# Optimization experiments

Measured on AMD Instinct MI355X. Metric: run time of the kernel, lower is better.

The kernel has to match this reference:

```python
import jax, jax.numpy as jnp
import numpy as np

HEAD_DIM = 16

def setup_inputs() -> dict:
    key = jax.random.key(0)
    ks = jax.random.split(key, 6)
    b, m, n, e, k, d = 2, 2048, 2048, 128, 8, HEAD_DIM
    # xavier-uniform-like scale for [e, d] fan
    s = float(np.sqrt(6.0 / (e + d)))
    return {
        "x": jax.random.normal(ks[0], (b, m, e), dtype=jnp.float32),
        "y": jax.random.normal(ks[1], (b, n, e), dtype=jnp.float32),
        "lambda1": jax.random.uniform(ks[2], (k, e, d), jnp.float32, -s, s),
        "lambda2": jax.random.uniform(ks[3], (k, e, d), jnp.float32, -s, s),
        "theta1": jax.random.uniform(ks[4], (k, e, d), jnp.float32, -s, s),
        "theta2": jax.random.uniform(ks[5], (k, e, d), jnp.float32, -s, s),
        "bias_lambda": jnp.zeros((k, d), jnp.float32),
        "bias_theta": jnp.zeros((k, d), jnp.float32),
    }

def reference(x, y, lambda1, lambda2, theta1, theta2, bias_lambda, bias_theta):
    head_dim = lambda1.shape[-1]
    # r: [b, m, k, d]
    r = jnp.einsum('bmp,kpd->bmkd', x, lambda1) + bias_lambda
    # dot_att: [k, b, m, n] (bilinear QK via per-head projections of x and y)
    dot_att = jnp.einsum('bmkd,kqd,bnq->kbmn', r, lambda2, y)
    dot_att = dot_att * (head_dim ** -0.5)
    # softmax over the query/m axis (-2), NOT the key axis
    att = jax.nn.softmax(dot_att, axis=-2)
    # combine: [b, n, k, d]
    r2 = jnp.einsum('kbmn,bmp,kpd->bnkd', att, x, theta1) + bias_theta
    # output: [b, n, emb_dim_x]
    return jnp.einsum('bnkd,kqd->bnq', r2, theta2)
```

## Files before the change

kernel.cpp:

```cpp
#include <hip/hip_runtime.h>
#include <math.h>

#define BB 2
#define MM 2048
#define NN 2048
#define EE 128
#define KH 8
#define DD 16
#define NHEADS (BB * KH)
#define MSPLIT 4
#define MCHUNK (MM / MSPLIT)

typedef __bf16 bf16x8 __attribute__((ext_vector_type(8)));
typedef __bf16 bf16x4 __attribute__((ext_vector_type(4)));
typedef float  f32x16 __attribute__((ext_vector_type(16)));
typedef float  f32x4  __attribute__((ext_vector_type(4)));

__global__ __launch_bounds__(256) void proj_kernel(
    const float* __restrict__ x, const float* __restrict__ y,
    const float* __restrict__ lambda1, const float* __restrict__ lambda2,
    const float* __restrict__ theta1, const float* __restrict__ bias_lambda,
    __bf16* __restrict__ rK, __bf16* __restrict__ kyQ, __bf16* __restrict__ Vt)
{
    __shared__ float xs[16][132];
    __shared__ float Ws[128][16];
    __shared__ float ts[16][17];

    const int tile = blockIdx.x;
    const int mt = tile & 127;
    const int k  = (tile >> 7) & 7;
    const int b  = tile >> 10;
    const int f  = blockIdx.y;
    const int tid = threadIdx.x;
    const int head = b * KH + k;

    const float* src = (f == 2) ? y : x;
    const float* W   = (f == 0) ? lambda1 : ((f == 1) ? theta1 : lambda2);

    const float* sp = src + ((size_t)b * MM + (size_t)mt * 16) * EE;
    for (int i = tid; i < 512; i += 256) {
        float4 v = ((const float4*)sp)[i];
        int row = i >> 5, cp = (i & 31) * 4;
        *(float4*)&xs[row][cp] = v;
    }
    const float* wp = W + (size_t)k * (EE * DD);
    for (int i = tid; i < 512; i += 256) {
        float4 v = ((const float4*)wp)[i];
        int row = i >> 2, cp = (i & 3) * 4;
        *(float4*)&Ws[row][cp] = v;
    }
    __syncthreads();

    const int row = tid >> 4, col = tid & 15;
    float acc = (f == 0) ? bias_lambda[k * DD + col] : 0.0f;
    #pragma unroll 16
    for (int p = 0; p < EE; ++p)
        acc = fmaf(xs[row][p], Ws[p][col], acc);

    const int m = mt * 16 + row;
    if (f == 0) {
        rK[((size_t)head * MM + m) * DD + col] = (__bf16)acc;
    } else if (f == 2) {
        kyQ[((size_t)head * NN + m) * DD + col] = (__bf16)(acc * 0.25f);
    } else {
        ts[col][row] = acc;
        __syncthreads();
        const int dd2 = tid >> 4, mloc = tid & 15;
        Vt[((size_t)head * DD + dd2) * MM + mt * 16 + mloc] = (__bf16)ts[dd2][mloc];
    }
}

__global__ __launch_bounds__(256) void attn_kernel(
    const __bf16* __restrict__ rK, const __bf16* __restrict__ kyQ,
    const __bf16* __restrict__ Vt,
    float* __restrict__ Opart, float* __restrict__ mlP)
{
    __shared__ __bf16 Pst[4][32][40];

    const int tid  = threadIdx.x;
    const int wave = tid >> 6;
    const int lane = tid & 63;
    const int head = blockIdx.x >> 4;
    const int nbase = (blockIdx.x & 15) * 128 + wave * 32;
    const int ms   = blockIdx.y;

    const int l31 = lane & 31;
    const int hi  = lane >> 5;
    const int l15 = lane & 15;
    const int g4  = lane >> 4;

    const bf16x8 qf = *reinterpret_cast<const bf16x8*>(
        kyQ + ((size_t)head * NN + nbase + l31) * DD + 8 * hi);

    f32x4 o0, o1;
    #pragma unroll
    for (int i = 0; i < 4; ++i) { o0[i] = 0.f; o1[i] = 0.f; }
    float mmax = -INFINITY, lsum = 0.f;

    const __bf16* kb = rK + (size_t)head * MM * DD;
    const __bf16* vb = Vt + (size_t)head * DD * MM;

    for (int it = 0; it < MCHUNK / 32; ++it) {
        const int m0 = ms * MCHUNK + it * 32;

        const bf16x8 kf = *reinterpret_cast<const bf16x8*>(
            kb + ((size_t)(m0 + l31)) * DD + 8 * hi);

        f32x16 s;
        #pragma unroll
        for (int i = 0; i < 16; ++i) s[i] = 0.f;
        s = __builtin_amdgcn_mfma_f32_32x32x16_bf16(kf, qf, s, 0, 0, 0);

        float tm = s[0];
        #pragma unroll
        for (int r = 1; r < 16; ++r) tm = fmaxf(tm, s[r]);
        tm = fmaxf(tm, __shfl_xor(tm, 32));
        const float newm = fmaxf(mmax, tm);
        const float c = __expf(mmax - newm);

        float p[16];
        float ps = 0.f;
        #pragma unroll
        for (int r = 0; r < 16; ++r) { p[r] = __expf(s[r] - newm); ps += p[r]; }
        ps += __shfl_xor(ps, 32);
        lsum = lsum * c + ps;
        mmax = newm;

        #pragma unroll
        for (int qd = 0; qd < 4; ++qd) {
            bf16x4 pk;
            pk[0] = (__bf16)p[4 * qd + 0];
            pk[1] = (__bf16)p[4 * qd + 1];
            pk[2] = (__bf16)p[4 * qd + 2];
            pk[3] = (__bf16)p[4 * qd + 3];
            *reinterpret_cast<bf16x4*>(&Pst[wave][l31][8 * qd + 4 * hi]) = pk;
        }

        const bf16x8 vf = *reinterpret_cast<const bf16x8*>(
            vb + (size_t)l15 * MM + m0 + 8 * g4);

        const bf16x8 pa0 = *reinterpret_cast<const bf16x8*>(&Pst[wave][l15][8 * g4]);
        const bf16x8 pa1 = *reinterpret_cast<const bf16x8*>(&Pst[wave][16 + l15][8 * g4]);

        #pragma unroll
        for (int r = 0; r < 4; ++r) {
            const float c0 = __shfl(c, 4 * g4 + r);
            const float c1 = __shfl(c, 16 + 4 * g4 + r);
            o0[r] *= c0;
            o1[r] *= c1;
        }
        o0 = __builtin_amdgcn_mfma_f32_16x16x32_bf16(pa0, vf, o0, 0, 0, 0);
        o1 = __builtin_amdgcn_mfma_f32_16x16x32_bf16(pa1, vf, o1, 0, 0, 0);
    }

    float* obase = Opart + ((size_t)ms * NHEADS + head) * NN * DD;
    #pragma unroll
    for (int r = 0; r < 4; ++r) {
        const int n0 = nbase + 4 * g4 + r;
        const int n1 = n0 + 16;
        obase[(size_t)n0 * DD + l15] = o0[r];
        obase[(size_t)n1 * DD + l15] = o1[r];
    }
    if (lane < 32) {
        const size_t mlbase = (((size_t)ms * NHEADS + head) * NN + nbase + l31) * 2;
        mlP[mlbase]     = mmax;
        mlP[mlbase + 1] = lsum;
    }
}

__global__ __launch_bounds__(256) void combine_kernel(
    const float* __restrict__ Opart, const float* __restrict__ mlP,
    const float* __restrict__ bias_theta, const float* __restrict__ theta2,
    float* __restrict__ out)
{
    __shared__ float r2s[2][128];

    const int pairIdx = blockIdx.x;
    const int b   = pairIdx >> 10;
    const int np0 = (pairIdx & 1023) * 2;
    const int tid = threadIdx.x;

    {
        const int n_loc = tid >> 7;
        const int rem = tid & 127;
        const int k = rem >> 4, dd = rem & 15;
        const int n = np0 + n_loc;
        const int head = b * KH + k;

        float mm[MSPLIT], ls[MSPLIT];
        float Mx = -INFINITY;
        #pragma unroll
        for (int s2 = 0; s2 < MSPLIT; ++s2) {
            const size_t base = ((size_t)s2 * NHEADS + head) * NN + n;
            mm[s2] = mlP[base * 2];
            ls[s2] = mlP[base * 2 + 1];
            Mx = fmaxf(Mx, mm[s2]);
        }
        float L = 0.f, O = 0.f;
        #pragma unroll
        for (int s2 = 0; s2 < MSPLIT; ++s2) {
            const float w = __expf(mm[s2] - Mx);
            L += ls[s2] * w;
            O = fmaf(Opart[(((size_t)s2 * NHEADS + head) * NN + n) * DD + dd], w, O);
        }
        r2s[n_loc][rem] = O / L + bias_theta[k * DD + dd];
    }
    __syncthreads();
    {
        const int n_loc = tid >> 7;
        const int qq = tid & 127;
        const int n = np0 + n_loc;
        float acc = 0.f;
        #pragma unroll
        for (int k = 0; k < KH; ++k) {
            const float4* t2 = (const float4*)(theta2 + ((size_t)k * EE + qq) * DD);
            const float* r2p = &r2s[n_loc][k * DD];
            float4 t0 = t2[0], t1 = t2[1], t2v = t2[2], t3 = t2[3];
            acc = fmaf(r2p[0],  t0.x, acc); acc = fmaf(r2p[1],  t0.y, acc);
            acc = fmaf(r2p[2],  t0.z, acc); acc = fmaf(r2p[3],  t0.w, acc);
            acc = fmaf(r2p[4],  t1.x, acc); acc = fmaf(r2p[5],  t1.y, acc);
            acc = fmaf(r2p[6],  t1.z, acc); acc = fmaf(r2p[7],  t1.w, acc);
            acc = fmaf(r2p[8],  t2v.x, acc); acc = fmaf(r2p[9],  t2v.y, acc);
            acc = fmaf(r2p[10], t2v.z, acc); acc = fmaf(r2p[11], t2v.w, acc);
            acc = fmaf(r2p[12], t3.x, acc); acc = fmaf(r2p[13], t3.y, acc);
            acc = fmaf(r2p[14], t3.z, acc); acc = fmaf(r2p[15], t3.w, acc);
        }
        out[((size_t)b * NN + n) * EE + qq] = acc;
    }
}

extern "C" void kernel_launch(void* const* d_in, const int* in_sizes, int n_in,
                              void* d_out, int out_size, void* d_ws, size_t ws_size,
                              hipStream_t stream) {
    const float* x           = (const float*)d_in[0];
    const float* y           = (const float*)d_in[1];
    const float* lambda1     = (const float*)d_in[2];
    const float* lambda2     = (const float*)d_in[3];
    const float* theta1      = (const float*)d_in[4];
    const float* theta2      = (const float*)d_in[5];
    const float* bias_lambda = (const float*)d_in[6];
    const float* bias_theta  = (const float*)d_in[7];
    float* out = (float*)d_out;

    char* w = (char*)d_ws;
    __bf16* rK  = (__bf16*)w;  w += (size_t)NHEADS * MM * DD * 2;
    __bf16* kyQ = (__bf16*)w;  w += (size_t)NHEADS * NN * DD * 2;
    __bf16* Vt  = (__bf16*)w;  w += (size_t)NHEADS * DD * MM * 2;
    float* Opart = (float*)w;  w += (size_t)MSPLIT * NHEADS * NN * DD * 4;
    float* mlP   = (float*)w;

    hipLaunchKernelGGL(proj_kernel, dim3(2048, 3), dim3(256), 0, stream,
                       x, y, lambda1, lambda2, theta1, bias_lambda, rK, kyQ, Vt);
    hipLaunchKernelGGL(attn_kernel, dim3(256, MSPLIT), dim3(256), 0, stream,
                       rK, kyQ, Vt, Opart, mlP);
    hipLaunchKernelGGL(combine_kernel, dim3(2048), dim3(256), 0, stream,
                       Opart, mlP, bias_theta, theta2, out);
}
```

Measured before the change: 130.9 us.

## Rewrite projection with MFMA, defer softmax rescale, double M-split, relayout partials

The projection kernel now runs on bf16 MFMA instructions, with each wave handling several 16-row tiles, replacing the scalar LDS FMA loop. The attention kernel uses exp2 with log2e folded into the query scale. It also skips rescaling the running max and accumulators unless the new max exceeds the old by more than a threshold. MSPLIT goes from 4 to 8 for more parallelism, and the partial outputs are relaid out as [split, b, n, k, d] so the combine kernel can use float4 loads and handle four rows per block. Risks: bf16 rounding of x and the weights in the projection, a deferred max that lets exponents reach up to 2^8, and twice as much partial-output traffic.

After: 116.3 us. 11.2% less time.

```diff
diff --git a/kernel.cpp b/kernel.cpp
--- a/kernel.cpp
+++ b/kernel.cpp
@@ -8,13 +8,23 @@
 #define KH 8
 #define DD 16
 #define NHEADS (BB * KH)
-#define MSPLIT 4
+#define MSPLIT 8
 #define MCHUNK (MM / MSPLIT)
+#define LOG2E 1.44269504088896340736f
+#define QSCALE (0.25f * LOG2E)
+#define DEFER_THR 8.0f
 
 typedef __bf16 bf16x8 __attribute__((ext_vector_type(8)));
 typedef __bf16 bf16x4 __attribute__((ext_vector_type(4)));
 typedef float  f32x16 __attribute__((ext_vector_type(16)));
 typedef float  f32x4  __attribute__((ext_vector_type(4)));
+
+__device__ inline bf16x8 cvt8(float4 a, float4 b) {
+    bf16x8 r;
+    r[0] = (__bf16)a.x; r[1] = (__bf16)a.y; r[2] = (__bf16)a.z; r[3] = (__bf16)a.w;
+    r[4] = (__bf16)b.x; r[5] = (__bf16)b.y; r[6] = (__bf16)b.z; r[7] = (__bf16)b.w;
+    return r;
+}
 
 __global__ __launch_bounds__(256) void proj_kernel(
     const float* __restrict__ x, const float* __restrict__ y,
@@ -22,51 +32,59 @@
     const float* __restrict__ theta1, const float* __restrict__ bias_lambda,
     __bf16* __restrict__ rK, __bf16* __restrict__ kyQ, __bf16* __restrict__ Vt)
 {
-    __shared__ float xs[16][132];
-    __shared__ float Ws[128][16];
-    __shared__ float ts[16][17];
-
-    const int tile = blockIdx.x;
-    const int mt = tile & 127;
-    const int k  = (tile >> 7) & 7;
-    const int b  = tile >> 10;
-    const int f  = blockIdx.y;
-    const int tid = threadIdx.x;
-    const int head = b * KH + k;
-
-    const float* src = (f == 2) ? y : x;
-    const float* W   = (f == 0) ? lambda1 : ((f == 1) ? theta1 : lambda2);
-
-    const float* sp = src + ((size_t)b * MM + (size_t)mt * 16) * EE;
-    for (int i = tid; i < 512; i += 256) {
-        float4 v = ((const float4*)sp)[i];
-        int row = i >> 5, cp = (i & 31) * 4;
-        *(float4*)&xs[row][cp] = v;
-    }
-    const float* wp = W + (size_t)k * (EE * DD);
-    for (int i = tid; i < 512; i += 256) {
-        float4 v = ((const float4*)wp)[i];
-        int row = i >> 2, cp = (i & 3) * 4;
-        *(float4*)&Ws[row][cp] = v;
-    }
-    __syncthreads();
-
-    const int row = tid >> 4, col = tid & 15;
-    float acc = (f == 0) ? bias_lambda[k * DD + col] : 0.0f;
-    #pragma unroll 16
-    for (int p = 0; p < EE; ++p)
-        acc = fmaf(xs[row][p], Ws[p][col], acc);
-
-    const int m = mt * 16 + row;
-    if (f == 0) {
-        rK[((size_t)head * MM + m) * DD + col] = (__bf16)acc;
-    } else if (f == 2) {
-        kyQ[((size_t)head * NN + m) * DD + col] = (__bf16)(acc * 0.25f);
-    } else {
-        ts[col][row] = acc;
-        __syncthreads();
-        const int dd2 = tid >> 4, mloc = tid & 15;
-        Vt[((size_t)head * DD + dd2) * MM + mt * 16 + mloc] = (__bf16)ts[dd2][mloc];
+    const int grp  = blockIdx.x;
+    const int f    = blockIdx.y;
+    const int head = blockIdx.z;
+    const int b = head >> 3, kh = head & 7;
+    const int wave = threadIdx.x >> 6;
+    const int lane = threadIdx.x & 63;
+    const int l15 = lane & 15, g4 = lane >> 4;
+
+    const float* W   = ((f == 0) ? lambda1 : (f == 1) ? theta1 : lambda2)
+                       + (size_t)kh * EE * DD;
+    const float* src = ((f == 2) ? y : x) + (size_t)b * MM * EE;
+
+    bf16x8 wf[4];
+    #pragma unroll
+    for (int kb = 0; kb < 4; ++kb) {
+        const float* wp = W + (size_t)(32 * kb + 8 * g4) * DD + l15;
+        bf16x8 t;
+        #pragma unroll
+        for (int e = 0; e < 8; ++e) t[e] = (__bf16)wp[e * DD];
+        wf[kb] = t;
+    }
+    const float bl = (f == 0) ? bias_lambda[kh * DD + l15] : 0.f;
+
+    for (int i = 0; i < 4; ++i) {
+        const int m0 = (grp * 16 + wave * 4 + i) * 16;
+        const float* xp = src + (size_t)(m0 + l15) * EE + 8 * g4;
+
+        f32x4 acc;
+        #pragma unroll
+        for (int r = 0; r < 4; ++r) acc[r] = 0.f;
+
+        #pragma unroll
+        for (int kb = 0; kb < 4; ++kb) {
+            float4 a = *(const float4*)(xp + 32 * kb);
+            float4 c = *(const float4*)(xp + 32 * kb + 4);
+            bf16x8 xf = cvt8(a, c);
+            if (f == 1) acc = __builtin_amdgcn_mfma_f32_16x16x32_bf16(wf[kb], xf, acc, 0, 0, 0);
+            else        acc = __builtin_amdgcn_mfma_f32_16x16x32_bf16(xf, wf[kb], acc, 0, 0, 0);
+        }
+
+        if (f == 0) {
+            #pragma unroll
+            for (int r = 0; r < 4; ++r)
+                rK[((size_t)head * MM + m0 + 4 * g4 + r) * DD + l15] = (__bf16)(acc[r] + bl);
+        } else if (f == 2) {
+            #pragma unroll
+            for (int r = 0; r < 4; ++r)
+                kyQ[((size_t)head * NN + m0 + 4 * g4 + r) * DD + l15] = (__bf16)(acc[r] * QSCALE);
+        } else {
+            #pragma unroll
+            for (int r = 0; r < 4; ++r)
+                Vt[((size_t)head * DD + 4 * g4 + r) * MM + m0 + l15] = (__bf16)acc[r];
+        }
     }
 }
 
@@ -83,6 +101,7 @@
     const int head = blockIdx.x >> 4;
     const int nbase = (blockIdx.x & 15) * 128 + wave * 32;
     const int ms   = blockIdx.y;
+    const int b = head >> 3, kh = head & 7;
 
     const int l31 = lane & 31;
     const int hi  = lane >> 5;
@@ -115,16 +134,25 @@
         #pragma unroll
         for (int r = 1; r < 16; ++r) tm = fmaxf(tm, s[r]);
         tm = fmaxf(tm, __shfl_xor(tm, 32));
-        const float newm = fmaxf(mmax, tm);
-        const float c = __expf(mmax - newm);
+
+        if (!__all(tm - mmax <= DEFER_THR)) {
+            const float newm = fmaxf(mmax, tm);
+            const float c = exp2f(mmax - newm);
+            lsum *= c;
+            #pragma unroll
+            for (int r = 0; r < 4; ++r) {
+                o0[r] *= __shfl(c, 4 * g4 + r);
+                o1[r] *= __shfl(c, 16 + 4 * g4 + r);
+            }
+            mmax = newm;
+        }
 
         float p[16];
         float ps = 0.f;
         #pragma unroll
-        for (int r = 0; r < 16; ++r) { p[r] = __expf(s[r] - newm); ps += p[r]; }
+        for (int r = 0; r < 16; ++r) { p[r] = exp2f(s[r] - mmax); ps += p[r]; }
         ps += __shfl_xor(ps, 32);
-        lsum = lsum * c + ps;
-        mmax = newm;
+        lsum += ps;
 
         #pragma unroll
         for (int qd = 0; qd < 4; ++qd) {
@@ -142,27 +170,20 @@
         const bf16x8 pa0 = *reinterpret_cast<const bf16x8*>(&Pst[wave][l15][8 * g4]);
         const bf16x8 pa1 = *reinterpret_cast<const bf16x8*>(&Pst[wave][16 + l15][8 * g4]);
 
-        #pragma unroll
-        for (int r = 0; r < 4; ++r) {
-            const float c0 = __shfl(c, 4 * g4 + r);
-            const float c1 = __shfl(c, 16 + 4 * g4 + r);
-            o0[r] *= c0;
-            o1[r] *= c1;
-        }
         o0 = __builtin_amdgcn_mfma_f32_16x16x32_bf16(pa0, vf, o0, 0, 0, 0);
         o1 = __builtin_amdgcn_mfma_f32_16x16x32_bf16(pa1, vf, o1, 0, 0, 0);
     }
 
-    float* obase = Opart + ((size_t)ms * NHEADS + head) * NN * DD;
+    float* obase = Opart + (((size_t)ms * BB + b) * NN) * (KH * DD) + kh * DD;
     #pragma unroll
     for (int r = 0; r < 4; ++r) {
         const int n0 = nbase + 4 * g4 + r;
         const int n1 = n0 + 16;
-        obase[(size_t)n0 * DD + l15] = o0[r];
-        obase[(size_t)n1 * DD + l15] = o1[r];
+        obase[(size_t)n0 * (KH * DD) + l15] = o0[r];
+        obase[(size_t)n1 * (KH * DD) + l15] = o1[r];
     }
     if (lane < 32) {
-        const size_t mlbase = (((size_t)ms * NHEADS + head) * NN + nbase + l31) * 2;
+        const size_t mlbase = (((size_t)ms * BB + b) * NN + nbase + l31) * (KH * 2) + kh * 2;
         mlP[mlbase]     = mmax;
         mlP[mlbase + 1] = lsum;
     }
@@ -173,59 +194,71 @@
     const float* __restrict__ bias_theta, const float* __restrict__ theta2,
     float* __restrict__ out)
 {
-    __shared__ float r2s[2][128];
-
-    const int pairIdx = blockIdx.x;
-    const int b   = pairIdx >> 10;
-    const int np0 = (pairIdx & 1023) * 2;
+    __shared__ float r2s[4][128];
+
+    const int blk = blockIdx.x;
+    const int b   = blk >> 9;
+    const int n0  = (blk & 511) * 4;
     const int tid = threadIdx.x;
 
-    {
-        const int n_loc = tid >> 7;
-        const int rem = tid & 127;
-        const int k = rem >> 4, dd = rem & 15;
-        const int n = np0 + n_loc;
-        const int head = b * KH + k;
+    if (tid < 128) {
+        const int n_loc = tid >> 5;
+        const int k  = (tid >> 2) & 7;
+        const int dq = tid & 3;
+        const int n = n0 + n_loc;
 
         float mm[MSPLIT], ls[MSPLIT];
         float Mx = -INFINITY;
         #pragma unroll
-        for (int s2 = 0; s2 < MSPLIT; ++s2) {
-            const size_t base = ((size_t)s2 * NHEADS + head) * NN + n;
-            mm[s2] = mlP[base * 2];
-            ls[s2] = mlP[base * 2 + 1];
-            Mx = fmaxf(Mx, mm[s2]);
-        }
-        float L = 0.f, O = 0.f;
-        #pragma unroll
-        for (int s2 = 0; s2 < MSPLIT; ++s2) {
-            const float w = __expf(mm[s2] - Mx);
-            L += ls[s2] * w;
-            O = fmaf(Opart[(((size_t)s2 * NHEADS + head) * NN + n) * DD + dd], w, O);
-        }
-        r2s[n_loc][rem] = O / L + bias_theta[k * DD + dd];
+        for (int s = 0; s < MSPLIT; ++s) {
+            const size_t base = (((size_t)s * BB + b) * NN + n) * (KH * 2) + k * 2;
+            mm[s] = mlP[base];
+            ls[s] = mlP[base + 1];
+            Mx = fmaxf(Mx, mm[s]);
+        }
+        float L = 0.f;
+        float4 O = make_float4(0.f, 0.f, 0.f, 0.f);
+        #pragma unroll
+        for (int s = 0; s < MSPLIT; ++s) {
+            const float w = exp2f(mm[s] - Mx);
+            L = fmaf(ls[s], w, L);
+            const float4 op = *(const float4*)(
+                Opart + (((size_t)s * BB + b) * NN + n) * (KH * DD) + k * DD + dq * 4);
+            O.x = fmaf(w, op.x, O.x); O.y = fmaf(w, op.y, O.y);
+            O.z = fmaf(w, op.z, O.z); O.w = fmaf(w, op.w, O.w);
+        }
+        const float inv = 1.f / L;
+        const float* bt = bias_theta + k * DD + dq * 4;
+        float4 res;
+        res.x = fmaf(O.x, inv, bt[0]);
+        res.y = fmaf(O.y, inv, bt[1]);
+        res.z = fmaf(O.z, inv, bt[2]);
+        res.w = fmaf(O.w, inv, bt[3]);
+        *(float4*)&r2s[n_loc][k * DD + dq * 4] = res;
     }
     __syncthreads();
     {
-        const int n_loc = tid >> 7;
-        const int qq = tid & 127;
-        const int n = np0 + n_loc;
-        float acc = 0.f;
+        const int q   = tid & 127;
+        const int nl0 = tid >> 7;
+        float acc0 = 0.f, acc1 = 0.f;
         #pragma unroll
         for (int k = 0; k < KH; ++k) {
-            const float4* t2 = (const float4*)(theta2 + ((size_t)k * EE + qq) * DD);
-            const float* r2p = &r2s[n_loc][k * DD];
-            float4 t0 = t2[0], t1 = t2[1], t2v = t2[2], t3 = t2[3];
-            acc = fmaf(r2p[0],  t0.x, acc); acc = fmaf(r2p[1],  t0.y, acc);
-            acc = fmaf(r2p[2],  t0.z, acc); acc = fmaf(r2p[3],  t0.w, acc);
-            acc = fmaf(r2p[4],  t1.x, acc); acc = fmaf(r2p[5],  t1.y, acc);
-            acc = fmaf(r2p[6],  t1.z, acc); acc = fmaf(r2p[7],  t1.w, acc);
-            acc = fmaf(r2p[8],  t2v.x, acc); acc = fmaf(r2p[9],  t2v.y, acc);
-            acc = fmaf(r2p[10], t2v.z, acc); acc = fmaf(r2p[11], t2v.w, acc);
-            acc = fmaf(r2p[12], t3.x, acc); acc = fmaf(r2p[13], t3.y, acc);
-            acc = fmaf(r2p[14], t3.z, acc); acc = fmaf(r2p[15], t3.w, acc);
-        }
-        out[((size_t)b * NN + n) * EE + qq] = acc;
+            const float4* t2 = (const float4*)(theta2 + ((size_t)k * EE + q) * DD);
+            const float4* ra = (const float4*)&r2s[nl0][k * DD];
+            const float4* rb = (const float4*)&r2s[nl0 + 2][k * DD];
+            #pragma unroll
+            for (int j = 0; j < 4; ++j) {
+                const float4 t = t2[j];
+                const float4 a = ra[j];
+                const float4 bq = rb[j];
+                acc0 = fmaf(a.x, t.x, acc0);  acc0 = fmaf(a.y, t.y, acc0);
+                acc0 = fmaf(a.z, t.z, acc0);  acc0 = fmaf(a.w, t.w, acc0);
+                acc1 = fmaf(bq.x, t.x, acc1); acc1 = fmaf(bq.y, t.y, acc1);
+                acc1 = fmaf(bq.z, t.z, acc1); acc1 = fmaf(bq.w, t.w, acc1);
+            }
+        }
+        out[((size_t)b * NN + n0 + nl0) * EE + q]     = acc0;
+        out[((size_t)b * NN + n0 + nl0 + 2) * EE + q] = acc1;
     }
 }
 
@@ -246,13 +279,13 @@
     __bf16* rK  = (__bf16*)w;  w += (size_t)NHEADS * MM * DD * 2;
     __bf16* kyQ = (__bf16*)w;  w += (size_t)NHEADS * NN * DD * 2;
     __bf16* Vt  = (__bf16*)w;  w += (size_t)NHEADS * DD * MM * 2;
-    float* Opart = (float*)w;  w += (size_t)MSPLIT * NHEADS * NN * DD * 4;
+    float* Opart = (float*)w;  w += (size_t)MSPLIT * BB * NN * KH * DD * 4;
     float* mlP   = (float*)w;
 
-    hipLaunchKernelGGL(proj_kernel, dim3(2048, 3), dim3(256), 0, stream,
+    hipLaunchKernelGGL(proj_kernel, dim3(8, 3, 16), dim3(256), 0, stream,
                        x, y, lambda1, lambda2, theta1, bias_lambda, rK, kyQ, Vt);
     hipLaunchKernelGGL(attn_kernel, dim3(256, MSPLIT), dim3(256), 0, stream,
                        rK, kyQ, Vt, Opart, mlP);
-    hipLaunchKernelGGL(combine_kernel, dim3(2048), dim3(256), 0, stream,
+    hipLaunchKernelGGL(combine_kernel, dim3(1024), dim3(256), 0, stream,
                        Opart, mlP, bias_theta, theta2, out);
 }
```
